# Kernel tuning notes

Hardware: AMD Instinct MI355X
Metric: run time of the kernel (lower is better)

## Reference

```python
import jax, jax.numpy as jnp
import numpy as np

N, E, G = 100000, 1600000, 1024
BN_EPS = 1e-5
NEG_SLOPE = 0.2


def setup_inputs() -> dict:
    key = jax.random.key(0)
    ks = jax.random.split(key, 8)
    x = jax.random.normal(ks[0], (N, 128), dtype=jnp.float32)
    edge_index = jax.random.randint(ks[1], (2, E), 0, N, dtype=jnp.int64)
    batch = jnp.sort(jax.random.randint(ks[2], (N,), 0, G, dtype=jnp.int64))
    Wl = jax.random.normal(ks[3], (3, 128, 128), dtype=jnp.float32) * 0.08
    bl = jnp.zeros((3, 128), dtype=jnp.float32)
    Wr = jax.random.normal(ks[4], (3, 128, 128), dtype=jnp.float32) * 0.08
    bn_gamma = jnp.ones((3, 128), dtype=jnp.float32)
    bn_beta = jnp.zeros((3, 128), dtype=jnp.float32)
    bn2_gamma = jnp.ones((128,), dtype=jnp.float32)
    bn2_beta = jnp.zeros((128,), dtype=jnp.float32)
    fc_W = jax.random.normal(ks[5], (128, 64), dtype=jnp.float32) * 0.08
    fc_b = jnp.zeros((64,), dtype=jnp.float32)
    return {"x": x, "edge_index": edge_index, "batch": batch, "Wl": Wl, "bl": bl,
            "Wr": Wr, "bn_gamma": bn_gamma, "bn_beta": bn_beta,
            "bn2_gamma": bn2_gamma, "bn2_beta": bn2_beta, "fc_W": fc_W, "fc_b": fc_b}


def _batch_norm(h, gamma, beta):
    # training-mode BatchNorm1d: batch statistics, biased variance
    mu = jnp.mean(h, axis=0)
    var = jnp.mean((h - mu) ** 2, axis=0)
    return gamma * (h - mu) * jax.lax.rsqrt(var + BN_EPS) + beta


def reference(x, edge_index, batch, Wl, bl, Wr, bn_gamma, bn_beta,
              bn2_gamma, bn2_beta, fc_W, fc_b):
    src, dst = edge_index[0], edge_index[1]
    # in-degree of each destination node (for mean aggregation)
    deg = jax.ops.segment_sum(jnp.ones((E,), dtype=x.dtype), dst, num_segments=N)
    inv_deg = jnp.where(deg > 0, 1.0 / jnp.maximum(deg, 1.0), 0.0)[:, None]  # [N,1]
    h = x
    for i in range(3):
        # SAGEConv: out = lin_l(mean_{j in N(i)} h_j) + lin_r(h_i)
        agg = jax.ops.segment_sum(h[src], dst, num_segments=N) * inv_deg  # [N,H]
        h = agg @ Wl[i] + bl[i] + h @ Wr[i]
        h = jax.nn.leaky_relu(_batch_norm(h, bn_gamma[i], bn_beta[i]), NEG_SLOPE)
        # dropout omitted (eval-mode / deterministic reference)
    pooled = jax.ops.segment_sum(h, batch, num_segments=G)  # [G,H] global_add_pool
    out = _batch_norm(pooled, bn2_gamma, bn2_beta) @ fc_W + fc_b  # [G,latent]
    return out
```

## Files before the change

### kernel.cpp

```cpp
#include <hip/hip_runtime.h>

#define HD 128
#define NCOPY 32
#define BSH 8
#define BSZ 256
#define EPB 4096

typedef __attribute__((ext_vector_type(8))) short short8;
typedef __attribute__((ext_vector_type(4))) float f32x4;

union ABu { unsigned long long u[2]; short8 s8; };

__device__ inline float bf2f(ushort u) {
    union { unsigned int i; float f; } x; x.i = ((unsigned int)u) << 16; return x.f;
}
__device__ inline float bflo(unsigned int u) {
    union { unsigned int i; float f; } x; x.i = u << 16; return x.f;
}
__device__ inline float bfhi(unsigned int u) {
    union { unsigned int i; float f; } x; x.i = u & 0xffff0000u; return x.f;
}
__device__ inline ushort f2bf(float f) {
    union { float f; unsigned int i; } x; x.f = f;
    unsigned int r = x.i + 0x7FFF + ((x.i >> 16) & 1);
    return (ushort)(r >> 16);
}


__global__ __launch_bounds__(256) void kp_count(const int* __restrict__ dst,
                                                int* __restrict__ bucketCount, int E, int NB) {
    __shared__ int hist[512];
    for (int i = threadIdx.x; i < NB; i += 256) hist[i] = 0;
    __syncthreads();
    int e0 = blockIdx.x * EPB;
#pragma unroll
    for (int j = 0; j < 16; ++j) {
        int e = e0 + j * 256 + threadIdx.x;
        if (e < E) atomicAdd(&hist[dst[e] >> BSH], 1);
    }
    __syncthreads();
    for (int i = threadIdx.x; i < NB; i += 256)
        if (hist[i]) atomicAdd(&bucketCount[i], hist[i]);
}

__global__ void kp_scan(const int* __restrict__ bucketCount, int* __restrict__ bucketBase,
                        int* __restrict__ gCursor, int NB, int E) {
    __shared__ int lds[512];
    int tid = threadIdx.x;
    int v = (tid < NB) ? bucketCount[tid] : 0;
    lds[tid] = v;
    __syncthreads();
    for (int off = 1; off < 512; off <<= 1) {
        int t = 0;
        if (tid >= off) t = lds[tid - off];
        __syncthreads();
        if (tid >= off) lds[tid] += t;
        __syncthreads();
    }
    int excl = lds[tid] - v;
    if (tid < NB) { bucketBase[tid] = excl; gCursor[tid] = excl; }
    if (tid == 0) bucketBase[NB] = E;
}

__global__ __launch_bounds__(256) void kp_part(const int* __restrict__ src,
                                               const int* __restrict__ dst,
                                               int* __restrict__ gCursor,
                                               unsigned int* __restrict__ packed, int E, int NB) {
    __shared__ int hist[512], lbase[512], lcur[512];
    for (int i = threadIdx.x; i < NB; i += 256) hist[i] = 0;
    __syncthreads();
    int e0 = blockIdx.x * EPB;
    int b[16]; unsigned int w[16];
#pragma unroll
    for (int j = 0; j < 16; ++j) {
        int e = e0 + j * 256 + threadIdx.x;
        b[j] = -1;
        if (e < E) {
            int d = dst[e];
            int s = src[e];
            b[j] = d >> BSH;
            w[j] = (unsigned int)s | (((unsigned int)d & (BSZ - 1)) << 17);
            atomicAdd(&hist[b[j]], 1);
        }
    }
    __syncthreads();
    for (int i = threadIdx.x; i < NB; i += 256) {
        int c = hist[i];
        lbase[i] = c ? atomicAdd(&gCursor[i], c) : 0;
        lcur[i] = 0;
    }
    __syncthreads();
#pragma unroll
    for (int j = 0; j < 16; ++j) {
        if (b[j] >= 0) {
            int r = atomicAdd(&lcur[b[j]], 1);
            packed[lbase[b[j]] + r] = w[j];
        }
    }
}

__global__ __launch_bounds__(256) void kp_degfill(const unsigned int* __restrict__ packed,
                                                  const int* __restrict__ bucketBase,
                                                  int* __restrict__ rowptr,
                                                  float* __restrict__ inv,
                                                  int* __restrict__ csr, int N, int E) {
    __shared__ int dcnt[BSZ];
    __shared__ int scn[BSZ];
    __shared__ int rp[BSZ];
    int bkt = blockIdx.x;
    int tid = threadIdx.x;
    int n0 = bkt << BSH;
    dcnt[tid] = 0;
    __syncthreads();
    int beg = bucketBase[bkt], end = bucketBase[bkt + 1];
    for (int e = beg + tid; e < end; e += 256)
        atomicAdd(&dcnt[packed[e] >> 17], 1);
    __syncthreads();
    int v = dcnt[tid];
    scn[tid] = v;
    __syncthreads();
    for (int off = 1; off < 256; off <<= 1) {
        int t = 0;
        if (tid >= off) t = scn[tid - off];
        __syncthreads();
        if (tid >= off) scn[tid] += t;
        __syncthreads();
    }
    int rpv = beg + scn[tid] - v;
    int n = n0 + tid;
    if (n < N) {
        rowptr[n] = rpv;
        inv[n] = (v > 0) ? (1.0f / (float)v) : 0.0f;
    }
    if (bkt == 0 && tid == 0) rowptr[N] = E;
    __syncthreads();
    dcnt[tid] = 0;
    rp[tid] = rpv;
    __syncthreads();
    for (int e = beg + tid; e < end; e += 256) {
        unsigned int wv = packed[e];
        int ld = wv >> 17;
        int p = atomicAdd(&dcnt[ld], 1);
        csr[rp[ld] + p] = (int)(wv & 0x1FFFF);
    }
}

__global__ void k_cvt(const float* __restrict__ in, ushort* __restrict__ out, int total4) {
    int i = blockIdx.x * blockDim.x + threadIdx.x;
    int stride = gridDim.x * blockDim.x;
    for (int idx = i; idx < total4; idx += stride) {
        float4 v = ((const float4*)in)[idx];
        ushort4 o;
        o.x = f2bf(v.x); o.y = f2bf(v.y); o.z = f2bf(v.z); o.w = f2bf(v.w);
        ((ushort4*)out)[idx] = o;
    }
}

__global__ void k_wt(const float* __restrict__ Wl, const float* __restrict__ Wr,
                     ushort* __restrict__ WT, int total) {
    int i = blockIdx.x * blockDim.x + threadIdx.x;
    if (i >= total) return;
    int l = i >> 15;
    int rem = i & 32767;
    int col = rem >> 8;
    int k = rem & 255;
    float v = (k < 128) ? Wl[l * 16384 + k * 128 + col] : Wr[l * 16384 + (k - 128) * 128 + col];
    WT[i] = f2bf(v);
}

__global__ __launch_bounds__(256) void k_agg(const ushort* __restrict__ h,
                                             const int* __restrict__ rowptr,
                                             const int* __restrict__ csr,
                                             const float* __restrict__ inv,
                                             ushort* __restrict__ agg, int N) {
    int node = blockIdx.x * 4 + (threadIdx.x >> 6);
    if (node >= N) return;
    int lane = threadIdx.x & 63;
    int g = lane >> 4, ln = lane & 15;
    int beg = rowptr[node], end = rowptr[node + 1];
    float a[8], b[8];
#pragma unroll
    for (int j = 0; j < 8; ++j) { a[j] = 0.f; b[j] = 0.f; }
    for (int e = beg + g; e < end; e += 8) {
        int s0 = csr[e];
        uint4 v0 = *(const uint4*)&h[(size_t)s0 * HD + ln * 8];
        int e1 = e + 4;
        if (e1 < end) {
            int s1 = csr[e1];
            uint4 v1 = *(const uint4*)&h[(size_t)s1 * HD + ln * 8];
            b[0] += bflo(v1.x); b[1] += bfhi(v1.x);
            b[2] += bflo(v1.y); b[3] += bfhi(v1.y);
            b[4] += bflo(v1.z); b[5] += bfhi(v1.z);
            b[6] += bflo(v1.w); b[7] += bfhi(v1.w);
        }
        a[0] += bflo(v0.x); a[1] += bfhi(v0.x);
        a[2] += bflo(v0.y); a[3] += bfhi(v0.y);
        a[4] += bflo(v0.z); a[5] += bfhi(v0.z);
        a[6] += bflo(v0.w); a[7] += bfhi(v0.w);
    }
#pragma unroll
    for (int j = 0; j < 8; ++j) {
        a[j] += b[j];
        a[j] += __shfl_xor(a[j], 16);
        a[j] += __shfl_xor(a[j], 32);
    }
    if (lane < 16) {
        float iv = inv[node];
        ushort o[8];
#pragma unroll
        for (int j = 0; j < 8; ++j) o[j] = f2bf(a[j] * iv);
        *(uint4*)&agg[(size_t)node * HD + ln * 8] = *(uint4*)o;
    }
}

__global__ __launch_bounds__(256) void k_gemm(
        const ushort* __restrict__ X1, const ushort* __restrict__ X2,
        const ushort* __restrict__ WT, const float* __restrict__ bias,
        ushort* __restrict__ out, float* __restrict__ stats, int N) {
    __shared__ ushort As[128 * 72];
    __shared__ ushort Bs[128 * 72];
    int tid = threadIdx.x;
    int lane = tid & 63, wid = tid >> 6;
    int wr = wid >> 1, wc = wid & 1;
    int ln15 = lane & 15, kg = lane >> 4;
    int rbase = blockIdx.x * 128;

    f32x4 acc[4][4];
#pragma unroll
    for (int m = 0; m < 4; ++m)
#pragma unroll
        for (int nn = 0; nn < 4; ++nn) acc[m][nn] = (f32x4){0.f, 0.f, 0.f, 0.f};

    for (int c = 0; c < 4; ++c) {
        const ushort* X = (c < 2) ? X1 : X2;
        int cb = (c & 1) * 64;
#pragma unroll
        for (int p = 0; p < 4; ++p) {
            int g = tid + p * 256;
            int r = g >> 3, q = g & 7;
            int grow = rbase + r;
            uint4 v = {0u, 0u, 0u, 0u};
            if (grow < N) v = *(const uint4*)&X[(size_t)grow * HD + cb + q * 8];
            *(uint4*)&As[r * 72 + q * 8] = v;
        }
#pragma unroll
        for (int p = 0; p < 4; ++p) {
            int g = tid + p * 256;
            int col = g >> 3, q = g & 7;
            *(uint4*)&Bs[col * 72 + q * 8] = *(const uint4*)&WT[col * 256 + c * 64 + q * 8];
        }
        __syncthreads();
#pragma unroll
        for (int kk = 0; kk < 2; ++kk) {
            short8 af[4], bfr[4];
#pragma unroll
            for (int m = 0; m < 4; ++m) {
                int row = wr * 64 + m * 16 + ln15;
                const ushort* pa = &As[row * 72 + kk * 32 + kg * 4];
                ABu u; u.u[0] = *(const unsigned long long*)pa;
                u.u[1] = *(const unsigned long long*)(pa + 16);
                af[m] = u.s8;
            }
#pragma unroll
            for (int nn = 0; nn < 4; ++nn) {
                int col = wc * 64 + nn * 16 + ln15;
                const ushort* pb = &Bs[col * 72 + kk * 32 + kg * 4];
                ABu u; u.u[0] = *(const unsigned long long*)pb;
                u.u[1] = *(const unsigned long long*)(pb + 16);
                bfr[nn] = u.s8;
            }
#pragma unroll
            for (int m = 0; m < 4; ++m)
#pragma unroll
                for (int nn = 0; nn < 4; ++nn)
                    acc[m][nn] = __builtin_amdgcn_mfma_f32_16x16x32_bf16(af[m], bfr[nn], acc[m][nn], 0, 0, 0);
        }
        __syncthreads();
    }

    float s[4] = {0.f, 0.f, 0.f, 0.f};
    float q[4] = {0.f, 0.f, 0.f, 0.f};
    float bv[4];
#pragma unroll
    for (int nn = 0; nn < 4; ++nn) bv[nn] = bias[wc * 64 + nn * 16 + ln15];
#pragma unroll
    for (int m = 0; m < 4; ++m) {
#pragma unroll
        for (int j = 0; j < 4; ++j) {
            int row = rbase + wr * 64 + m * 16 + kg * 4 + j;
            if (row < N) {
#pragma unroll
                for (int nn = 0; nn < 4; ++nn) {
                    float v = acc[m][nn][j] + bv[nn];
                    out[(size_t)row * HD + wc * 64 + nn * 16 + ln15] = f2bf(v);
                    s[nn] += v; q[nn] += v * v;
                }
            }
        }
    }
#pragma unroll
    for (int nn = 0; nn < 4; ++nn) {
        s[nn] += __shfl_xor(s[nn], 16); s[nn] += __shfl_xor(s[nn], 32);
        q[nn] += __shfl_xor(q[nn], 16); q[nn] += __shfl_xor(q[nn], 32);
    }
    if (lane < 16) {
        int slot = (blockIdx.x & (NCOPY - 1)) * 256;
#pragma unroll
        for (int nn = 0; nn < 4; ++nn) {
            int col = wc * 64 + nn * 16 + lane;
            atomicAdd(&stats[slot + col], s[nn]);
            atomicAdd(&stats[slot + 128 + col], q[nn]);
        }
    }
}

__global__ void k_bnfin(const float* __restrict__ stats, const float* __restrict__ gamma,
                        const float* __restrict__ beta, float* __restrict__ bnp, float count) {
    int c = threadIdx.x;
    float s = 0.f, q = 0.f;
    for (int i = 0; i < NCOPY; ++i) { s += stats[i * 256 + c]; q += stats[i * 256 + 128 + c]; }
    float mean = s / count;
    float var = q / count - mean * mean;
    var = fmaxf(var, 0.f);
    float scale = gamma[c] * rsqrtf(var + 1e-5f);
    bnp[c] = scale;
    bnp[128 + c] = beta[c] - mean * scale;
}

__global__ void k_apply(ushort* buf, const float* __restrict__ bnp, int total8) {
    int i = blockIdx.x * blockDim.x + threadIdx.x;
    int stride = gridDim.x * blockDim.x;
    for (int idx = i; idx < total8; idx += stride) {
        int cb = (idx * 8) & (HD - 1);
        uint4 v = ((const uint4*)buf)[idx];
        float f[8];
        f[0] = bflo(v.x); f[1] = bfhi(v.x);
        f[2] = bflo(v.y); f[3] = bfhi(v.y);
        f[4] = bflo(v.z); f[5] = bfhi(v.z);
        f[6] = bflo(v.w); f[7] = bfhi(v.w);
        ushort o[8];
#pragma unroll
        for (int j = 0; j < 8; ++j) {
            float y = f[j] * bnp[cb + j] + bnp[128 + cb + j];
            y = (y > 0.f) ? y : 0.2f * y;
            o[j] = f2bf(y);
        }
        ((uint4*)buf)[idx] = *(uint4*)o;
    }
}

__global__ void k_poolapply(const ushort* __restrict__ h, const float* __restrict__ bnp,
                            const int* __restrict__ batch, float* __restrict__ pooled, int N) {
    int c = threadIdx.x;
    float sc = bnp[c], sh = bnp[128 + c];
    int n0 = blockIdx.x * 16;
    if (n0 >= N) return;
    int nend = min(n0 + 16, N);
    float acc = 0.f;
    int cur = batch[n0];
    for (int n = n0; n < nend; ++n) {
        int b = batch[n];
        if (b != cur) { atomicAdd(&pooled[cur * HD + c], acc); acc = 0.f; cur = b; }
        float y = bf2f(h[(size_t)n * HD + c]) * sc + sh;
        y = (y > 0.f) ? y : 0.2f * y;
        acc += y;
    }
    atomicAdd(&pooled[cur * HD + c], acc);
}

__global__ void k_colstats(const float* __restrict__ X, float* __restrict__ stats, int rows) {
    int c = threadIdx.x;
    float s = 0.f, q = 0.f;
    for (int r = blockIdx.x; r < rows; r += gridDim.x) {
        float v = X[r * HD + c];
        s += v; q += v * v;
    }
    int slot = (blockIdx.x & (NCOPY - 1)) * 256;
    atomicAdd(&stats[slot + c], s);
    atomicAdd(&stats[slot + 128 + c], q);
}

__global__ void k_final(const float* __restrict__ pooled, const float* __restrict__ bnp,
                        const float* __restrict__ fcW, const float* __restrict__ fcb,
                        float* __restrict__ outp, int G) {
    __shared__ float Wlds[HD * 64];
    __shared__ float prow[HD];
    int tid = threadIdx.x;
    for (int i = tid; i < HD * 64 / 4; i += 64) ((float4*)Wlds)[i] = ((const float4*)fcW)[i];
    int g = blockIdx.x;
    for (int c = tid; c < HD; c += 64) prow[c] = pooled[g * HD + c] * bnp[c] + bnp[128 + c];
    __syncthreads();
    float acc = fcb[tid];
#pragma unroll 8
    for (int c = 0; c < HD; ++c) acc += prow[c] * Wlds[c * 64 + tid];
    outp[g * 64 + tid] = acc;
}

extern "C" void kernel_launch(void* const* d_in, const int* in_sizes, int n_in,
                              void* d_out, int out_size, void* d_ws, size_t ws_size,
                              hipStream_t stream) {
    const float* x     = (const float*)d_in[0];
    const int*   ei    = (const int*)d_in[1];
    const int*   batch = (const int*)d_in[2];
    const float* Wl    = (const float*)d_in[3];
    const float* bl    = (const float*)d_in[4];
    const float* Wr    = (const float*)d_in[5];
    const float* bng   = (const float*)d_in[6];
    const float* bnb   = (const float*)d_in[7];
    const float* bn2g  = (const float*)d_in[8];
    const float* bn2b  = (const float*)d_in[9];
    const float* fcW   = (const float*)d_in[10];
    const float* fcb   = (const float*)d_in[11];

    int N = in_sizes[0] / HD;
    int E = in_sizes[1] / 2;
    int G = out_size / 64;
    const int* src = ei;
    const int* dst = ei + E;

    char* p = (char*)d_ws;
    auto alloc = [&](size_t bytes) -> void* {
        void* r = (void*)p;
        p += (bytes + 255) & ~(size_t)255;
        return r;
    };
    int NB = (N + BSZ - 1) >> BSH;
    int nPB = (E + EPB - 1) / EPB;

    int*    rowptr   = (int*)alloc((size_t)(N + 1) * 4);
    int*    bCount   = (int*)alloc((size_t)NB * 4);
    int*    bBase    = (int*)alloc((size_t)(NB + 1) * 4);
    int*    gCursor  = (int*)alloc((size_t)NB * 4);
    int*    csr      = (int*)alloc((size_t)E * 4);
    float*  inv      = (float*)alloc((size_t)N * 4);
    ushort* WT       = (ushort*)alloc((size_t)3 * 128 * 256 * 2);
    ushort* xb       = (ushort*)alloc((size_t)N * HD * 2);
    ushort* aggb     = (ushort*)alloc((size_t)N * HD * 2);
    ushort* hb1      = (ushort*)alloc((size_t)N * HD * 2);
    ushort* hb2      = (ushort*)alloc((size_t)N * HD * 2);
    float*  statsAll = (float*)alloc((size_t)3 * NCOPY * 256 * 4);
    float*  stats2   = (float*)alloc((size_t)NCOPY * 256 * 4);
    float*  bnp      = (float*)alloc(256 * 4);
    float*  pooled   = (float*)alloc((size_t)G * HD * 4);

    float* stats0 = statsAll;
    float* stats1 = statsAll + NCOPY * 256;
    float* statsL2 = statsAll + 2 * NCOPY * 256;

    unsigned int* packed = (unsigned int*)aggb;

    float* outp = (float*)d_out;
    int total4 = N * HD / 4;
    int total8 = N * HD / 8;
    int ggrid = (N + 127) / 128;
    int agrid = (N + 3) / 4;

    hipMemsetAsync(statsAll, 0, (size_t)3 * NCOPY * 256 * 4, stream);
    hipMemsetAsync(stats2, 0, (size_t)NCOPY * 256 * 4, stream);
    hipMemsetAsync(pooled, 0, (size_t)G * HD * 4, stream);
    hipMemsetAsync(bCount, 0, (size_t)NB * 4, stream);
    k_cvt<<<2048, 256, 0, stream>>>(x, xb, total4);
    k_wt<<<(3 * 128 * 256 + 255) / 256, 256, 0, stream>>>(Wl, Wr, WT, 3 * 128 * 256);

    kp_count<<<nPB, 256, 0, stream>>>(dst, bCount, E, NB);
    kp_scan<<<1, 512, 0, stream>>>(bCount, bBase, gCursor, NB, E);
    kp_part<<<nPB, 256, 0, stream>>>(src, dst, gCursor, packed, E, NB);
    kp_degfill<<<NB, 256, 0, stream>>>(packed, bBase, rowptr, inv, csr, N, E);

    k_agg<<<agrid, 256, 0, stream>>>(xb, rowptr, csr, inv, aggb, N);
    k_gemm<<<ggrid, 256, 0, stream>>>(aggb, xb, WT, bl, hb1, stats0, N);
    k_bnfin<<<1, 128, 0, stream>>>(stats0, bng, bnb, bnp, (float)N);
    k_apply<<<2048, 256, 0, stream>>>(hb1, bnp, total8);

    k_agg<<<agrid, 256, 0, stream>>>(hb1, rowptr, csr, inv, aggb, N);
    k_gemm<<<ggrid, 256, 0, stream>>>(aggb, hb1, WT + 32768, bl + 128, hb2, stats1, N);
    k_bnfin<<<1, 128, 0, stream>>>(stats1, bng + 128, bnb + 128, bnp, (float)N);
    k_apply<<<2048, 256, 0, stream>>>(hb2, bnp, total8);

    k_agg<<<agrid, 256, 0, stream>>>(hb2, rowptr, csr, inv, aggb, N);
    k_gemm<<<ggrid, 256, 0, stream>>>(aggb, hb2, WT + 65536, bl + 256, hb1, statsL2, N);
    k_bnfin<<<1, 128, 0, stream>>>(statsL2, bng + 256, bnb + 256, bnp, (float)N);
    k_poolapply<<<(N + 15) / 16, HD, 0, stream>>>(hb1, bnp, batch, pooled, N);

    k_colstats<<<64, HD, 0, stream>>>(pooled, stats2, G);
    k_bnfin<<<1, 128, 0, stream>>>(stats2, bn2g, bn2b, bnp, (float)G);
    k_final<<<G, 64, 0, stream>>>(pooled, bnp, fcW, fcb, outp, G);
}
```

Before: 411.4 us.

## Fold BN finalize into consumers, merge prep kernels, prefetch GEMM tiles

Removes the four single-block k_bnfin launches by recomputing the BN scale and shift inside k_apply, k_poolapply and k_final. It also merges the x conversion and weight transpose into one k_prep kernel and collapses three memsets into one contiguous memset. The GEMM now loads the next K-chunk into registers while computing on the current one. The risks are redundant per-block reduction over 32 stat copies in thousands of blocks and higher register pressure in the GEMM.

New measurement: 421.3 us. 2.4% more time.

```diff
diff --git a/kernel.cpp b/kernel.cpp
--- a/kernel.cpp
+++ b/kernel.cpp
@@ -145,27 +145,26 @@
     }
 }
 
-__global__ void k_cvt(const float* __restrict__ in, ushort* __restrict__ out, int total4) {
+__global__ void k_prep(const float* __restrict__ x, ushort* __restrict__ xb, int total4,
+                       const float* __restrict__ Wl, const float* __restrict__ Wr,
+                       ushort* __restrict__ WT, int wtTotal) {
     int i = blockIdx.x * blockDim.x + threadIdx.x;
     int stride = gridDim.x * blockDim.x;
     for (int idx = i; idx < total4; idx += stride) {
-        float4 v = ((const float4*)in)[idx];
+        float4 v = ((const float4*)x)[idx];
         ushort4 o;
         o.x = f2bf(v.x); o.y = f2bf(v.y); o.z = f2bf(v.z); o.w = f2bf(v.w);
-        ((ushort4*)out)[idx] = o;
-    }
-}
-
-__global__ void k_wt(const float* __restrict__ Wl, const float* __restrict__ Wr,
-                     ushort* __restrict__ WT, int total) {
-    int i = blockIdx.x * blockDim.x + threadIdx.x;
-    if (i >= total) return;
-    int l = i >> 15;
-    int rem = i & 32767;
-    int col = rem >> 8;
-    int k = rem & 255;
-    float v = (k < 128) ? Wl[l * 16384 + k * 128 + col] : Wr[l * 16384 + (k - 128) * 128 + col];
-    WT[i] = f2bf(v);
+        ((ushort4*)xb)[idx] = o;
+    }
+    for (int idx = i; idx < wtTotal; idx += stride) {
+        int l = idx >> 15;
+        int rem = idx & 32767;
+        int col = rem >> 8;
+        int k = rem & 255;
+        float v = (k < 128) ? Wl[l * 16384 + k * 128 + col]
+                            : Wr[l * 16384 + (k - 128) * 128 + col];
+        WT[idx] = f2bf(v);
+    }
 }
 
 __global__ __launch_bounds__(256) void k_agg(const ushort* __restrict__ h,
@@ -224,6 +223,7 @@
     int wr = wid >> 1, wc = wid & 1;
     int ln15 = lane & 15, kg = lane >> 4;
     int rbase = blockIdx.x * 128;
+    int r0 = tid >> 3, q8 = (tid & 7) * 8;
 
     f32x4 acc[4][4];
 #pragma unroll
@@ -231,25 +231,31 @@
 #pragma unroll
         for (int nn = 0; nn < 4; ++nn) acc[m][nn] = (f32x4){0.f, 0.f, 0.f, 0.f};
 
-    for (int c = 0; c < 4; ++c) {
+    uint4 ra[4], rb[4];
+    auto loadchunk = [&](int c) {
         const ushort* X = (c < 2) ? X1 : X2;
         int cb = (c & 1) * 64;
 #pragma unroll
         for (int p = 0; p < 4; ++p) {
-            int g = tid + p * 256;
-            int r = g >> 3, q = g & 7;
+            int r = r0 + p * 32;
             int grow = rbase + r;
             uint4 v = {0u, 0u, 0u, 0u};
-            if (grow < N) v = *(const uint4*)&X[(size_t)grow * HD + cb + q * 8];
-            *(uint4*)&As[r * 72 + q * 8] = v;
-        }
+            if (grow < N) v = *(const uint4*)&X[(size_t)grow * HD + cb + q8];
+            ra[p] = v;
+            rb[p] = *(const uint4*)&WT[r * 256 + c * 64 + q8];
+        }
+    };
+    loadchunk(0);
+
+    for (int c = 0; c < 4; ++c) {
 #pragma unroll
         for (int p = 0; p < 4; ++p) {
-            int g = tid + p * 256;
-            int col = g >> 3, q = g & 7;
-            *(uint4*)&Bs[col * 72 + q * 8] = *(const uint4*)&WT[col * 256 + c * 64 + q * 8];
+            int r = r0 + p * 32;
+            *(uint4*)&As[r * 72 + q8] = ra[p];
+            *(uint4*)&Bs[r * 72 + q8] = rb[p];
         }
         __syncthreads();
+        if (c < 3) loadchunk(c + 1);
 #pragma unroll
         for (int kk = 0; kk < 2; ++kk) {
             short8 af[4], bfr[4];
@@ -314,21 +320,23 @@
     }
 }
 
-__global__ void k_bnfin(const float* __restrict__ stats, const float* __restrict__ gamma,
-                        const float* __restrict__ beta, float* __restrict__ bnp, float count) {
-    int c = threadIdx.x;
-    float s = 0.f, q = 0.f;
-    for (int i = 0; i < NCOPY; ++i) { s += stats[i * 256 + c]; q += stats[i * 256 + 128 + c]; }
-    float mean = s / count;
-    float var = q / count - mean * mean;
-    var = fmaxf(var, 0.f);
-    float scale = gamma[c] * rsqrtf(var + 1e-5f);
-    bnp[c] = scale;
-    bnp[128 + c] = beta[c] - mean * scale;
-}
-
-__global__ void k_apply(ushort* buf, const float* __restrict__ bnp, int total8) {
-    int i = blockIdx.x * blockDim.x + threadIdx.x;
+__global__ __launch_bounds__(256) void k_apply(ushort* buf, const float* __restrict__ stats,
+                                               const float* __restrict__ gamma,
+                                               const float* __restrict__ beta,
+                                               float count, int total8) {
+    __shared__ float sc[HD], sh[HD];
+    int tid = threadIdx.x;
+    if (tid < HD) {
+        float s = 0.f, q = 0.f;
+        for (int i = 0; i < NCOPY; ++i) { s += stats[i * 256 + tid]; q += stats[i * 256 + 128 + tid]; }
+        float mean = s / count;
+        float var = fmaxf(q / count - mean * mean, 0.f);
+        float scale = gamma[tid] * rsqrtf(var + 1e-5f);
+        sc[tid] = scale;
+        sh[tid] = beta[tid] - mean * scale;
+    }
+    __syncthreads();
+    int i = blockIdx.x * blockDim.x + tid;
     int stride = gridDim.x * blockDim.x;
     for (int idx = i; idx < total8; idx += stride) {
         int cb = (idx * 8) & (HD - 1);
@@ -341,7 +349,7 @@
         ushort o[8];
 #pragma unroll
         for (int j = 0; j < 8; ++j) {
-            float y = f[j] * bnp[cb + j] + bnp[128 + cb + j];
+            float y = f[j] * sc[cb + j] + sh[cb + j];
             y = (y > 0.f) ? y : 0.2f * y;
             o[j] = f2bf(y);
         }
@@ -349,10 +357,17 @@
     }
 }
 
-__global__ void k_poolapply(const ushort* __restrict__ h, const float* __restrict__ bnp,
-                            const int* __restrict__ batch, float* __restrict__ pooled, int N) {
+__global__ void k_poolapply(const ushort* __restrict__ h, const float* __restrict__ stats,
+                            const float* __restrict__ gamma, const float* __restrict__ beta,
+                            float count, const int* __restrict__ batch,
+                            float* __restrict__ pooled, int N) {
     int c = threadIdx.x;
-    float sc = bnp[c], sh = bnp[128 + c];
+    float s = 0.f, q = 0.f;
+    for (int i = 0; i < NCOPY; ++i) { s += stats[i * 256 + c]; q += stats[i * 256 + 128 + c]; }
+    float mean = s / count;
+    float var = fmaxf(q / count - mean * mean, 0.f);
+    float sc = gamma[c] * rsqrtf(var + 1e-5f);
+    float sh = beta[c] - mean * sc;
     int n0 = blockIdx.x * 16;
     if (n0 >= N) return;
     int nend = min(n0 + 16, N);
@@ -380,20 +395,29 @@
     atomicAdd(&stats[slot + 128 + c], q);
 }
 
-__global__ void k_final(const float* __restrict__ pooled, const float* __restrict__ bnp,
+__global__ void k_final(const float* __restrict__ pooled, const float* __restrict__ stats2,
+                        const float* __restrict__ bn2g, const float* __restrict__ bn2b,
                         const float* __restrict__ fcW, const float* __restrict__ fcb,
-                        float* __restrict__ outp, int G) {
+                        float* __restrict__ outp, float countG) {
     __shared__ float Wlds[HD * 64];
     __shared__ float prow[HD];
     int tid = threadIdx.x;
-    for (int i = tid; i < HD * 64 / 4; i += 64) ((float4*)Wlds)[i] = ((const float4*)fcW)[i];
+    for (int i = tid; i < HD * 64 / 4; i += 128) ((float4*)Wlds)[i] = ((const float4*)fcW)[i];
+    float s = 0.f, q = 0.f;
+    for (int i = 0; i < NCOPY; ++i) { s += stats2[i * 256 + tid]; q += stats2[i * 256 + 128 + tid]; }
+    float mean = s / countG;
+    float var = fmaxf(q / countG - mean * mean, 0.f);
+    float scale = bn2g[tid] * rsqrtf(var + 1e-5f);
+    float shift = bn2b[tid] - mean * scale;
     int g = blockIdx.x;
-    for (int c = tid; c < HD; c += 64) prow[c] = pooled[g * HD + c] * bnp[c] + bnp[128 + c];
-    __syncthreads();
-    float acc = fcb[tid];
+    prow[tid] = pooled[g * HD + tid] * scale + shift;
+    __syncthreads();
+    if (tid < 64) {
+        float acc = fcb[tid];
 #pragma unroll 8
-    for (int c = 0; c < HD; ++c) acc += prow[c] * Wlds[c * 64 + tid];
-    outp[g * 64 + tid] = acc;
+        for (int c = 0; c < HD; ++c) acc += prow[c] * Wlds[c * 64 + tid];
+        outp[g * 64 + tid] = acc;
+    }
 }
 
 extern "C" void kernel_launch(void* const* d_in, const int* in_sizes, int n_in,
@@ -438,14 +462,13 @@
     ushort* aggb     = (ushort*)alloc((size_t)N * HD * 2);
     ushort* hb1      = (ushort*)alloc((size_t)N * HD * 2);
     ushort* hb2      = (ushort*)alloc((size_t)N * HD * 2);
-    float*  statsAll = (float*)alloc((size_t)3 * NCOPY * 256 * 4);
-    float*  stats2   = (float*)alloc((size_t)NCOPY * 256 * 4);
-    float*  bnp      = (float*)alloc(256 * 4);
+    float*  statsAll = (float*)alloc((size_t)4 * NCOPY * 256 * 4);
     float*  pooled   = (float*)alloc((size_t)G * HD * 4);
 
-    float* stats0 = statsAll;
-    float* stats1 = statsAll + NCOPY * 256;
+    float* stats0  = statsAll;
+    float* stats1  = statsAll + NCOPY * 256;
     float* statsL2 = statsAll + 2 * NCOPY * 256;
+    float* stats2  = statsAll + 3 * NCOPY * 256;
 
     unsigned int* packed = (unsigned int*)aggb;
 
@@ -454,13 +477,11 @@
     int total8 = N * HD / 8;
     int ggrid = (N + 127) / 128;
     int agrid = (N + 3) / 4;
-
-    hipMemsetAsync(statsAll, 0, (size_t)3 * NCOPY * 256 * 4, stream);
-    hipMemsetAsync(stats2, 0, (size_t)NCOPY * 256 * 4, stream);
-    hipMemsetAsync(pooled, 0, (size_t)G * HD * 4, stream);
+    float fN = (float)N, fG = (float)G;
+
+    hipMemsetAsync(statsAll, 0, (size_t)4 * NCOPY * 256 * 4 + (size_t)G * HD * 4, stream);
     hipMemsetAsync(bCount, 0, (size_t)NB * 4, stream);
-    k_cvt<<<2048, 256, 0, stream>>>(x, xb, total4);
-    k_wt<<<(3 * 128 * 256 + 255) / 256, 256, 0, stream>>>(Wl, Wr, WT, 3 * 128 * 256);
+    k_prep<<<2048, 256, 0, stream>>>(x, xb, total4, Wl, Wr, WT, 3 * 128 * 256);
 
     kp_count<<<nPB, 256, 0, stream>>>(dst, bCount, E, NB);
     kp_scan<<<1, 512, 0, stream>>>(bCount, bBase, gCursor, NB, E);
@@ -469,20 +490,17 @@
 
     k_agg<<<agrid, 256, 0, stream>>>(xb, rowptr, csr, inv, aggb, N);
     k_gemm<<<ggrid, 256, 0, stream>>>(aggb, xb, WT, bl, hb1, stats0, N);
-    k_bnfin<<<1, 128, 0, stream>>>(stats0, bng, bnb, bnp, (float)N);
-    k_apply<<<2048, 256, 0, stream>>>(hb1, bnp, total8);
+    k_apply<<<2048, 256, 0, stream>>>(hb1, stats0, bng, bnb, fN, total8);
 
     k_agg<<<agrid, 256, 0, stream>>>(hb1, rowptr, csr, inv, aggb, N);
     k_gemm<<<ggrid, 256, 0, stream>>>(aggb, hb1, WT + 32768, bl + 128, hb2, stats1, N);
-    k_bnfin<<<1, 128, 0, stream>>>(stats1, bng + 128, bnb + 128, bnp, (float)N);
-    k_apply<<<2048, 256, 0, stream>>>(hb2, bnp, total8);
+    k_apply<<<2048, 256, 0, stream>>>(hb2, stats1, bng + 128, bnb + 128, fN, total8);
 
     k_agg<<<agrid, 256, 0, stream>>>(hb2, rowptr, csr, inv, aggb, N);
     k_gemm<<<ggrid, 256, 0, stream>>>(aggb, hb2, WT + 65536, bl + 256, hb1, statsL2, N);
-    k_bnfin<<<1, 128, 0, stream>>>(statsL2, bng + 256, bnb + 256, bnp, (float)N);
-    k_poolapply<<<(N + 15) / 16, HD, 0, stream>>>(hb1, bnp, batch, pooled, N);
+    k_poolapply<<<(N + 15) / 16, HD, 0, stream>>>(hb1, statsL2, bng + 256, bnb + 256, fN,
+                                                  batch, pooled, N);
 
     k_colstats<<<64, HD, 0, stream>>>(pooled, stats2, G);
-    k_bnfin<<<1, 128, 0, stream>>>(stats2, bn2g, bn2b, bnp, (float)G);
-    k_final<<<G, 64, 0, stream>>>(pooled, bnp, fcW, fcb, outp, G);
-}
+    k_final<<<G, HD, 0, stream>>>(pooled, stats2, bn2g, bn2b, fcW, fcb, outp, fG);
+}
```
